# Kernel tuning notes

Measured on AMD Instinct MI355X. Metric: run time of the kernel, lower is better.

## Reference

```python
import jax, jax.numpy as jnp
import numpy as np

D_MODEL = 256; N_HEADS = 8; D_FF = 1024; N_LAYERS = 8; N_BLOCKS = 4
VOCAB = 10000; N_SPARSE = 26; N_DENSE = 13; BATCH = 4096
SEQ = N_DENSE + N_SPARSE  # 39 feature tokens


def _ln(x, g, b, eps=1e-5):
    m = jnp.mean(x, -1, keepdims=True)
    v = jnp.mean((x - m) ** 2, -1, keepdims=True)
    return (x - m) * jax.lax.rsqrt(v + eps) * g + b


def _normalize(x, axis=-1, eps=1e-12):
    n = jnp.maximum(jnp.linalg.norm(x, axis=axis, keepdims=True), eps)
    return x / n


def setup_inputs() -> dict:
    key = jax.random.key(0)
    ks = iter(jax.random.split(key, 64))
    d, L, ff = D_MODEL, N_LAYERS, D_FF
    w = lambda shape: jax.random.normal(next(ks), shape, dtype=jnp.float32) * 0.02
    z = lambda shape: jnp.zeros(shape, jnp.float32)
    o = lambda shape: jnp.ones(shape, jnp.float32)
    return {
        "dense_x": jax.random.normal(next(ks), (BATCH, N_DENSE), dtype=jnp.float32),
        "sparse_x": jax.random.randint(next(ks), (BATCH, N_SPARSE), 0, VOCAB, dtype=jnp.int32),
        "W_dense": w((N_DENSE * d, N_DENSE)), "b_dense": z((N_DENSE * d,)),
        "emb": w((N_SPARSE, VOCAB + 1, d)),
        "Wq": w((L, d, d)), "bq": z((L, d)),
        "Wk": w((L, d, d)), "bk": z((L, d)),
        "Wv": w((L, d, d)), "bv": z((L, d)),
        "W1": w((L, ff, d)), "b1": z((L, ff)),
        "W2": w((L, d, ff)), "b2": z((L, d)),
        "n1g": o((L, d)), "n1b": z((L, d)),
        "n2g": o((L, d)), "n2b": z((L, d)),
        "qvec": w((N_BLOCKS, d)),
        "mha_in_w": w((3 * d, d)), "mha_in_b": z((3 * d,)),
        "mha_out_w": w((d, d)), "mha_out_b": z((d,)),
        "ng": o((d,)), "ngb": z((d,)),
        "Wo1": w((D_FF, SEQ * d)), "bo1": z((D_FF,)),
        "Wo2": w((1, D_FF)), "bo2": z((1,)),
    }


def reference(dense_x, sparse_x, W_dense, b_dense, emb, Wq, bq, Wk, bk, Wv, bv,
              W1, b1, W2, b2, n1g, n1b, n2g, n2b, qvec,
              mha_in_w, mha_in_b, mha_out_w, mha_out_b, ng, ngb,
              Wo1, bo1, Wo2, bo2):
    B = dense_x.shape[0]; d = D_MODEL; H = N_HEADS; dh = d // H
    # --- embed_features ---
    dense_emb = (dense_x @ W_dense.T + b_dense).reshape(B, N_DENSE, d)
    emb0 = emb.at[:, 0, :].set(0.0)  # padding_idx=0
    sp = emb0[jnp.arange(N_SPARSE), sparse_x]  # [B, 26, d]
    x = jnp.concatenate([dense_emb, sp], axis=1)  # [B, 39, d]

    scale = 1.0 / jnp.sqrt(jnp.float32(d))  # note: d_model, not head_dim
    block_size = N_LAYERS // N_BLOCKS
    block_outputs = [x]
    for i in range(N_LAYERS):
        # --- HSTU layer: sigmoid pointwise attention ---
        r = x
        h = _ln(x, n1g[i], n1b[i])
        q = (h @ Wq[i].T + bq[i]).reshape(B, SEQ, H, dh).transpose(0, 2, 1, 3)
        k = (h @ Wk[i].T + bk[i]).reshape(B, SEQ, H, dh).transpose(0, 2, 1, 3)
        v = (h @ Wv[i].T + bv[i]).reshape(B, SEQ, H, dh).transpose(0, 2, 1, 3)
        aw = jax.nn.sigmoid(jnp.einsum('bhqd,bhkd->bhqk', q, k) * scale)
        ao = jnp.einsum('bhqk,bhkd->bhqd', aw, v).transpose(0, 2, 1, 3).reshape(B, SEQ, d)
        x = r + ao
        r = x
        h = _ln(x, n2g[i], n2b[i])
        x = r + (jax.nn.relu(h @ W1[i].T + b1[i]) @ W2[i].T + b2[i])
        # --- AttentionResidual block mixing ---
        if (i + 1) % block_size == 0 and i < N_LAYERS - 1:
            V = jnp.stack(block_outputs + [x])  # [n, B, T, d]
            K = _normalize(V)
            qi = min(len(block_outputs), N_BLOCKS - 1)
            qn = _normalize(qvec[qi], axis=0)
            logits = jnp.einsum('d,nbtd->nbt', qn, K)
            wt = jax.nn.softmax(logits, axis=0)
            x = jnp.einsum('nbt,nbtd->btd', wt, V)
            block_outputs.append(x)

    # --- final LayerNorm + standard MHA residual ---
    r = x
    h = _ln(x, ng, ngb)
    qkv = h @ mha_in_w.T + mha_in_b
    q, k, v = jnp.split(qkv, 3, axis=-1)
    q = q.reshape(B, SEQ, H, dh).transpose(0, 2, 1, 3)
    k = k.reshape(B, SEQ, H, dh).transpose(0, 2, 1, 3)
    v = v.reshape(B, SEQ, H, dh).transpose(0, 2, 1, 3)
    at = jax.nn.softmax(jnp.einsum('bhqd,bhkd->bhqk', q, k) / jnp.sqrt(jnp.float32(dh)), axis=-1)
    mo = jnp.einsum('bhqk,bhkd->bhqd', at, v).transpose(0, 2, 1, 3).reshape(B, SEQ, d)
    x = r + (mo @ mha_out_w.T + mha_out_b)

    flat = x.reshape(B, -1)
    return (jax.nn.relu(flat @ Wo1.T + bo1) @ Wo2.T + bo2).squeeze(-1)
```

## Files before the change

### kernel.cpp

```cpp
#include <hip/hip_runtime.h>
#include <hip/hip_bf16.h>

typedef __attribute__((ext_vector_type(4))) float f32x4;
typedef __attribute__((ext_vector_type(8))) short short8;
typedef __attribute__((ext_vector_type(4))) unsigned short us4;

static __device__ __forceinline__ unsigned short f2bf(float f){
  return __builtin_bit_cast(unsigned short, __float2bfloat16(f));
}
static __device__ __forceinline__ float bf2f(unsigned short u){
  return __bfloat162float(__builtin_bit_cast(__hip_bfloat16, u));
}
static __device__ __forceinline__ short8 zero8(){
  short8 v;
#pragma unroll
  for (int e=0;e<8;++e) v[e]=0;
  return v;
}
static __device__ __forceinline__ void g2l16(const void* g, void* l){
  __builtin_amdgcn_global_load_lds(
    (const __attribute__((address_space(1))) unsigned int*)g,
    (__attribute__((address_space(3))) unsigned int*)l, 16, 0, 0);
}

template<int EPI>
__global__ __launch_bounds__(256)
void gemm_k(const unsigned short* __restrict__ Ap, int lda,
            const unsigned short* __restrict__ Bp,
            const float* __restrict__ bias,
            void* __restrict__ Outp, int ldo, int K,
            unsigned short* __restrict__ vT, int nColBlk)
{
  const int id = blockIdx.x;
  const int xcd = id & 7; const int t0 = id >> 3;
  const int cb = t0 % nColBlk; const int rb = (t0 / nColBlk)*8 + xcd;
  const long rowBase = (long)rb << 7;
  const long colBase = (long)cb << 7;
  const int tid = threadIdx.x, lane = tid & 63, w = tid >> 6;
  const int wm = (w >> 1) << 6, wn = (w & 1) << 6;
  const int cl = lane & 15, q4 = lane >> 4;

  __shared__ __align__(16) unsigned short As[128*64];
  __shared__ __align__(16) unsigned short Bs[128*64];

  const char* bSrc[4]; unsigned short* bDst[4];
  const char* aSrc[4]; unsigned short* aDst[4];
#pragma unroll
  for (int g=0; g<4; ++g){
    const int c = (w<<8) + (g<<6) + lane;
    const int r = c>>3, x = c&7, c16 = x ^ (r&7);
    bSrc[g] = (const char*)(Bp + (colBase + r)*(long)K) + c16*16;
    bDst[g] = Bs + (((w<<2)+g)<<9);
    aSrc[g] = (const char*)(Ap + (rowBase + r)*(long)lda) + c16*16;
    aDst[g] = As + (((w<<2)+g)<<9);
  }

  f32x4 acc[4][4];
#pragma unroll
  for (int m=0;m<4;++m)
#pragma unroll
    for (int n=0;n<4;++n) acc[m][n] = (f32x4){0.f,0.f,0.f,0.f};

  const int nk = K >> 6;
  for (int t=0; t<nk; ++t){
    if (t) __syncthreads();
    const long tb = (long)t << 7;
#pragma unroll
    for (int g=0; g<4; ++g){
      g2l16(bSrc[g] + tb, bDst[g]);
      g2l16(aSrc[g] + tb, aDst[g]);
    }
    __syncthreads();
#pragma unroll
    for (int ks=0; ks<2; ++ks){
      const int kb = ks*64 + (q4<<4);
      short8 af[4], bf_[4];
#pragma unroll
      for (int m=0;m<4;++m){
        const int r = wm + m*16 + cl;
        af[m] = *(const short8*)((const char*)As + r*128 + (kb ^ ((r&7)<<4)));
      }
#pragma unroll
      for (int n=0;n<4;++n){
        const int r = wn + n*16 + cl;
        bf_[n] = *(const short8*)((const char*)Bs + r*128 + (kb ^ ((r&7)<<4)));
      }
#pragma unroll
      for (int m=0;m<4;++m)
#pragma unroll
        for (int n=0;n<4;++n)
          acc[m][n] = __builtin_amdgcn_mfma_f32_16x16x32_bf16(af[m], bf_[n], acc[m][n], 0,0,0);
    }
  }

#pragma unroll
  for (int n=0;n<4;++n){
    const long col = colBase + wn + n*16 + cl;
    const float bi = bias[col];
#pragma unroll
    for (int m=0;m<4;++m){
      const long r0 = rowBase + wm + m*16 + (q4<<2);
#pragma unroll
      for (int i=0;i<4;++i){
        const float v = acc[m][n][i] + bi;
        const long row = r0 + i;
        if constexpr (EPI == 1){
          ((unsigned short*)Outp)[row*(long)ldo + col] = f2bf(fmaxf(v,0.f));
        } else {
          if (col < 512){
            ((unsigned short*)Outp)[row*512 + col] = f2bf(v);
          } else {
            const int bb = (int)row / 39;
            const int tt = (int)row - bb*39;
            unsigned short* vrow = vT + ((long)bb*256 + (col - 512))*48;
            vrow[tt] = f2bf(v);
            if (tt < 9) vrow[tt + 39] = 0;
          }
        }
      }
    }
  }
}

__global__ __launch_bounds__(512)
void ffn_k(const float* __restrict__ xf_in,
           const float* __restrict__ sB, const float* __restrict__ cB,
           const unsigned short* __restrict__ W1p,
           const float* __restrict__ b1p,
           const unsigned short* __restrict__ W2p,
           const float* __restrict__ b2p,
           float* __restrict__ xf,
           unsigned short* __restrict__ xln1)
{
  __shared__ __align__(16) unsigned short Wb1[64*256];
  __shared__ __align__(16) unsigned short Wb2[256*64];
  __shared__ __align__(16) unsigned short Hs[128*64];
  float* part1 = (float*)Wb1;
  float* part2 = part1 + 512;
  float* sln   = part2 + 512;
  float* cln   = sln + 128;

  const int tid = threadIdx.x, lane = tid & 63, w = tid >> 6;
  const int cl = lane & 15, q4 = lane >> 4;
  const long rowBase = (long)blockIdx.x << 7;
  const int wm = (w >> 2) << 6, wn = (w & 3) << 6;

  short8 af[8];
  {
    const int row = (w<<4) + cl;
    const float s = sB[rowBase + row], c = cB[rowBase + row];
    const float* src = xf_in + (rowBase + row)*256 + (q4<<3);
#pragma unroll
    for (int kt=0; kt<8; ++kt){
      f32x4 a = *(const f32x4*)(src + kt*32);
      f32x4 b = *(const f32x4*)(src + kt*32 + 4);
      short8 v;
#pragma unroll
      for (int e=0;e<4;++e){ v[e] = (short)f2bf(a[e]*s + c); v[4+e] = (short)f2bf(b[e]*s + c); }
      af[kt] = v;
    }
  }

  f32x4 acc[4][4];
#pragma unroll
  for (int m=0;m<4;++m)
#pragma unroll
    for (int n=0;n<4;++n) acc[m][n] = (f32x4){0.f,0.f,0.f,0.f};

  for (int j=0; j<16; ++j){
    const int ffbase = j<<6;
    __syncthreads();
#pragma unroll
    for (int it=0; it<4; ++it){
      const int g = tid + (it<<9);
      {
        const int kt = g>>9, cc = g&511, rr = cc>>3, xs = cc&7;
        g2l16(W1p + ((long)(ffbase+rr))*256 + (kt<<6) + ((xs^(rr&7))<<3),
              Wb1 + (((tid & ~63) + (it<<9))<<3));
      }
      {
        const int rr = g>>3, xs = g&7;
        g2l16(W2p + (long)rr*1024 + ffbase + ((xs^(rr&7))<<3),
              Wb2 + (((tid & ~63) + (it<<9))<<3));
      }
    }
    float b1v[4];
#pragma unroll
    for (int n=0;n<4;++n) b1v[n] = b1p[ffbase + n*16 + cl];
    __syncthreads();

    f32x4 hacc[4];
#pragma unroll
    for (int n=0;n<4;++n) hacc[n] = (f32x4){0.f,0.f,0.f,0.f};
#pragma unroll
    for (int kt2=0; kt2<4; ++kt2)
#pragma unroll
      for (int ks=0; ks<2; ++ks){
        const int kb = ks*64 + (q4<<4);
        const short8 a = af[kt2*2 + ks];
#pragma unroll
        for (int n=0;n<4;++n){
          const int rn = n*16 + cl;
          short8 bf_ = *(const short8*)((const char*)Wb1 + (kt2<<13) + rn*128 + (kb ^ ((rn&7)<<4)));
          hacc[n] = __builtin_amdgcn_mfma_f32_16x16x32_bf16(a, bf_, hacc[n], 0,0,0);
        }
      }
#pragma unroll
    for (int n=0;n<4;++n)
#pragma unroll
      for (int i=0;i<4;++i){
        const int hr = (w<<4) + (q4<<2) + i, hc = n*16 + cl;
        const float hv = fmaxf(hacc[n][i] + b1v[n], 0.f);
        *(unsigned short*)((char*)Hs + hr*128 + ((hc*2) ^ ((hr&7)<<4))) = f2bf(hv);
      }
    __syncthreads();

#pragma unroll
    for (int ks=0; ks<2; ++ks){
      const int kb = ks*64 + (q4<<4);
      short8 am[4], bm[4];
#pragma unroll
      for (int m=0;m<4;++m){
        const int r = wm + m*16 + cl;
        am[m] = *(const short8*)((const char*)Hs + r*128 + (kb ^ ((r&7)<<4)));
      }
#pragma unroll
      for (int n=0;n<4;++n){
        const int r = wn + n*16 + cl;
        bm[n] = *(const short8*)((const char*)Wb2 + r*128 + (kb ^ ((r&7)<<4)));
      }
#pragma unroll
      for (int m=0;m<4;++m)
#pragma unroll
        for (int n=0;n<4;++n)
          acc[m][n] = __builtin_amdgcn_mfma_f32_16x16x32_bf16(am[m], bm[n], acc[m][n], 0,0,0);
    }
  }

#pragma unroll
  for (int n=0;n<4;++n){
    const int col = wn + n*16 + cl;
    const float bi = b2p[col];
#pragma unroll
    for (int m=0;m<4;++m)
#pragma unroll
      for (int i=0;i<4;++i){
        const int row = wm + m*16 + (q4<<2) + i;
        const long gi = (rowBase + row)*256 + col;
        const float v = acc[m][n][i] + bi + xf[gi];
        acc[m][n][i] = v;
        xf[gi] = v;
      }
  }
  __syncthreads();
#pragma unroll
  for (int m=0;m<4;++m)
#pragma unroll
    for (int i=0;i<4;++i){
      float s1 = 0.f, s2 = 0.f;
#pragma unroll
      for (int n=0;n<4;++n){ const float v = acc[m][n][i]; s1 += v; s2 += v*v; }
#pragma unroll
      for (int off=8; off; off>>=1){ s1 += __shfl_xor(s1, off, 16); s2 += __shfl_xor(s2, off, 16); }
      const int row = wm + m*16 + (q4<<2) + i;
      if (cl == 0){ part1[row*4 + (w&3)] = s1; part2[row*4 + (w&3)] = s2; }
    }
  __syncthreads();
  if (tid < 128){
    const float S1 = part1[tid*4]+part1[tid*4+1]+part1[tid*4+2]+part1[tid*4+3];
    const float S2 = part2[tid*4]+part2[tid*4+1]+part2[tid*4+2]+part2[tid*4+3];
    const float mn = S1*(1.f/256.f);
    const float var = S2*(1.f/256.f) - mn*mn;
    const float s = rsqrtf(var + 1e-5f);
    sln[tid] = s; cln[tid] = -mn*s;
  }
  __syncthreads();
#pragma unroll
  for (int m=0;m<4;++m)
#pragma unroll
    for (int i=0;i<4;++i){
      const int row = wm + m*16 + (q4<<2) + i;
      const float s = sln[row], c = cln[row];
#pragma unroll
      for (int n=0;n<4;++n){
        const int col = wn + n*16 + cl;
        xln1[(rowBase + row)*256 + col] = f2bf(acc[m][n][i]*s + c);
      }
    }
}

__global__ __launch_bounds__(256)
void attn_sig_k(const unsigned short* __restrict__ qkb,
                const unsigned short* __restrict__ vT,
                float* xf, float* __restrict__ sB, float* __restrict__ cB)
{
  __shared__ __align__(16) unsigned short Ps[4*48*64];
  __shared__ float part[312];

  const int b = blockIdx.x;
  const int tid = threadIdx.x, lane = tid & 63, w = tid >> 6;
  const int cl = lane & 15, q4 = lane >> 4;
  unsigned short* P = Ps + w*3072;
  const unsigned short* qb = qkb + (long)b*39*512;
  const unsigned short* vbb = vT + (long)b*256*48;

  if (lane < 48){
    const int r = lane;
    *(short8*)((char*)P + r*128 + (96  ^ ((r&7)<<4))) = zero8();
    *(short8*)((char*)P + r*128 + (112 ^ ((r&7)<<4))) = zero8();
  }

  float ps1[3][4], ps2[3][4];
#pragma unroll
  for (int m=0;m<3;++m)
#pragma unroll
    for (int i=0;i<4;++i){ ps1[m][i]=0.f; ps2[m][i]=0.f; }

#pragma unroll
  for (int hh=0; hh<2; ++hh){
    const int h = (w<<1) + hh;
    f32x4 sac[3][3];
#pragma unroll
    for (int m=0;m<3;++m)
#pragma unroll
      for (int n=0;n<3;++n) sac[m][n] = (f32x4){0.f,0.f,0.f,0.f};
    short8 aq[3], bk8[3];
#pragma unroll
    for (int m=0;m<3;++m){
      const int r = m*16 + cl;
      aq[m] = (r < 39) ? *(const short8*)(qb + (long)r*512 + h*32 + q4*8) : zero8();
    }
#pragma unroll
    for (int n=0;n<3;++n){
      const int r = n*16 + cl;
      bk8[n] = (r < 39) ? *(const short8*)(qb + (long)r*512 + 256 + h*32 + q4*8) : zero8();
    }
#pragma unroll
    for (int m=0;m<3;++m)
#pragma unroll
      for (int n=0;n<3;++n)
        sac[m][n] = __builtin_amdgcn_mfma_f32_16x16x32_bf16(aq[m], bk8[n], sac[m][n], 0,0,0);
#pragma unroll
    for (int m=0;m<3;++m)
#pragma unroll
      for (int n=0;n<3;++n)
#pragma unroll
        for (int i=0;i<4;++i){
          const int row = m*16 + (q4<<2) + i, col = n*16 + cl;
          const float pv = 1.f/(1.f + __expf(-sac[m][n][i]*0.0625f));
          *(unsigned short*)((char*)P + row*128 + ((col*2) ^ ((row&7)<<4))) = f2bf(pv);
        }
    f32x4 aoc[3][2];
#pragma unroll
    for (int m=0;m<3;++m)
#pragma unroll
      for (int n=0;n<2;++n) aoc[m][n] = (f32x4){0.f,0.f,0.f,0.f};
#pragma unroll
    for (int ks=0; ks<2; ++ks){
      const int kb = ks*64 + (q4<<4);
      short8 pa[3], vb[2];
#pragma unroll
      for (int m=0;m<3;++m){
        const int r = m*16 + cl;
        pa[m] = *(const short8*)((const char*)P + r*128 + (kb ^ ((r&7)<<4)));
      }
#pragma unroll
      for (int n=0;n<2;++n){
        vb[n] = zero8();
        if (ks == 0 || q4 < 2)
          vb[n] = *(const short8*)(vbb + (long)(h*32 + n*16 + cl)*48 + ks*32 + q4*8);
      }
#pragma unroll
      for (int m=0;m<3;++m)
#pragma unroll
        for (int n=0;n<2;++n)
          aoc[m][n] = __builtin_amdgcn_mfma_f32_16x16x32_bf16(pa[m], vb[n], aoc[m][n], 0,0,0);
    }
#pragma unroll
    for (int m=0;m<3;++m)
#pragma unroll
      for (int n=0;n<2;++n)
#pragma unroll
        for (int i=0;i<4;++i){
          const int row = m*16 + (q4<<2) + i;
          if (row < 39){
            const long gi = (((long)(b*39+row))<<8) + h*32 + n*16 + cl;
            const float nv = xf[gi] + aoc[m][n][i];
            xf[gi] = nv;
            ps1[m][i] += nv; ps2[m][i] += nv*nv;
          }
        }
  }
#pragma unroll
  for (int m=0;m<3;++m)
#pragma unroll
    for (int i=0;i<4;++i){
      float a1 = ps1[m][i], a2 = ps2[m][i];
#pragma unroll
      for (int off=8; off; off>>=1){ a1 += __shfl_xor(a1, off, 16); a2 += __shfl_xor(a2, off, 16); }
      const int row = m*16 + (q4<<2) + i;
      if (cl == 0 && row < 39){ part[row*8 + (w<<1)] = a1; part[row*8 + (w<<1) + 1] = a2; }
    }
  __syncthreads();
  if (tid < 39){
    const float S1 = part[tid*8]+part[tid*8+2]+part[tid*8+4]+part[tid*8+6];
    const float S2 = part[tid*8+1]+part[tid*8+3]+part[tid*8+5]+part[tid*8+7];
    const float mn = S1*(1.f/256.f);
    const float var = S2*(1.f/256.f) - mn*mn;
    const float s = rsqrtf(var + 1e-5f);
    sB[b*39+tid] = s; cB[b*39+tid] = -mn*s;
  }
}

__global__ __launch_bounds__(256)
void attn_fin_k(const unsigned short* __restrict__ qkb,
                const unsigned short* __restrict__ vT,
                const float* __restrict__ xf,
                const unsigned short* __restrict__ moW,
                const float* __restrict__ moB,
                unsigned short* __restrict__ flatb)
{
  __shared__ __align__(16) unsigned short Ps[4*48*64];
  __shared__ __align__(16) unsigned short Mo[48*256];

  const int b = blockIdx.x;
  const int tid = threadIdx.x, lane = tid & 63, w = tid >> 6;
  const int cl = lane & 15, q4 = lane >> 4;
  unsigned short* P = Ps + w*3072;
  const unsigned short* qb = qkb + (long)b*39*512;
  const unsigned short* vbb = vT + (long)b*256*48;
  const float SC = 0.17677669529663687f;

  if (lane < 48){
    const int r = lane;
    *(short8*)((char*)P + r*128 + (96  ^ ((r&7)<<4))) = zero8();
    *(short8*)((char*)P + r*128 + (112 ^ ((r&7)<<4))) = zero8();
  }

#pragma unroll
  for (int hh=0; hh<2; ++hh){
    const int h = (w<<1) + hh;
    f32x4 sac[3][3];
#pragma unroll
    for (int m=0;m<3;++m)
#pragma unroll
      for (int n=0;n<3;++n) sac[m][n] = (f32x4){0.f,0.f,0.f,0.f};
    short8 aq[3], bk8[3];
#pragma unroll
    for (int m=0;m<3;++m){
      const int r = m*16 + cl;
      aq[m] = (r < 39) ? *(const short8*)(qb + (long)r*512 + h*32 + q4*8) : zero8();
    }
#pragma unroll
    for (int n=0;n<3;++n){
      const int r = n*16 + cl;
      bk8[n] = (r < 39) ? *(const short8*)(qb + (long)r*512 + 256 + h*32 + q4*8) : zero8();
    }
#pragma unroll
    for (int m=0;m<3;++m)
#pragma unroll
      for (int n=0;n<3;++n)
        sac[m][n] = __builtin_amdgcn_mfma_f32_16x16x32_bf16(aq[m], bk8[n], sac[m][n], 0,0,0);
#pragma unroll
    for (int m=0;m<3;++m)
#pragma unroll
      for (int i=0;i<4;++i){
        const float v0 = sac[m][0][i]*SC, v1 = sac[m][1][i]*SC, v2 = sac[m][2][i]*SC;
        const bool c2ok = (32 + cl) < 39;
        float mx = fmaxf(v0, v1);
        if (c2ok) mx = fmaxf(mx, v2);
#pragma unroll
        for (int off=8; off; off>>=1) mx = fmaxf(mx, __shfl_xor(mx, off, 16));
        const float e0 = __expf(v0-mx), e1 = __expf(v1-mx);
        const float e2 = c2ok ? __expf(v2-mx) : 0.f;
        float s = e0+e1+e2;
#pragma unroll
        for (int off=8; off; off>>=1) s += __shfl_xor(s, off, 16);
        const float inv = 1.f/s;
        const int row = m*16 + (q4<<2) + i;
        *(unsigned short*)((char*)P + row*128 + (((cl   )*2) ^ ((row&7)<<4))) = f2bf(e0*inv);
        *(unsigned short*)((char*)P + row*128 + (((16+cl)*2) ^ ((row&7)<<4))) = f2bf(e1*inv);
        *(unsigned short*)((char*)P + row*128 + (((32+cl)*2) ^ ((row&7)<<4))) = f2bf(e2*inv);
      }
    f32x4 aoc[3][2];
#pragma unroll
    for (int m=0;m<3;++m)
#pragma unroll
      for (int n=0;n<2;++n) aoc[m][n] = (f32x4){0.f,0.f,0.f,0.f};
#pragma unroll
    for (int ks=0; ks<2; ++ks){
      const int kb = ks*64 + (q4<<4);
      short8 pa[3], vb[2];
#pragma unroll
      for (int m=0;m<3;++m){
        const int r = m*16 + cl;
        pa[m] = *(const short8*)((const char*)P + r*128 + (kb ^ ((r&7)<<4)));
      }
#pragma unroll
      for (int n=0;n<2;++n){
        vb[n] = zero8();
        if (ks == 0 || q4 < 2)
          vb[n] = *(const short8*)(vbb + (long)(h*32 + n*16 + cl)*48 + ks*32 + q4*8);
      }
#pragma unroll
      for (int m=0;m<3;++m)
#pragma unroll
        for (int n=0;n<2;++n)
          aoc[m][n] = __builtin_amdgcn_mfma_f32_16x16x32_bf16(pa[m], vb[n], aoc[m][n], 0,0,0);
    }
#pragma unroll
    for (int m=0;m<3;++m)
#pragma unroll
      for (int n=0;n<2;++n)
#pragma unroll
        for (int i=0;i<4;++i){
          const int row = m*16 + (q4<<2) + i;
          const int colq = h*32 + n*16 + cl;
          *(unsigned short*)((char*)Mo + row*512 + ((colq*2) ^ ((row&7)<<4))) = f2bf(aoc[m][n][i]);
        }
  }
  __syncthreads();
  f32x4 oc[3][4];
#pragma unroll
  for (int m=0;m<3;++m)
#pragma unroll
    for (int n=0;n<4;++n) oc[m][n] = (f32x4){0.f,0.f,0.f,0.f};
#pragma unroll
  for (int ks=0; ks<8; ++ks){
    const int kb = ks*64 + (q4<<4);
    short8 am[3], bm[4];
#pragma unroll
    for (int m=0;m<3;++m){
      const int r = m*16 + cl;
      am[m] = *(const short8*)((const char*)Mo + r*512 + (kb ^ ((r&7)<<4)));
    }
#pragma unroll
    for (int n=0;n<4;++n){
      const int nn = (w<<6) + n*16 + cl;
      bm[n] = *(const short8*)(moW + (long)nn*256 + ks*32 + q4*8);
    }
#pragma unroll
    for (int m=0;m<3;++m)
#pragma unroll
      for (int n=0;n<4;++n)
        oc[m][n] = __builtin_amdgcn_mfma_f32_16x16x32_bf16(am[m], bm[n], oc[m][n], 0,0,0);
  }
#pragma unroll
  for (int m=0;m<3;++m)
#pragma unroll
    for (int n=0;n<4;++n)
#pragma unroll
      for (int i=0;i<4;++i){
        const int row = m*16 + (q4<<2) + i;
        if (row < 39){
          const int col = (w<<6) + n*16 + cl;
          const float v = oc[m][n][i] + moB[col] + xf[(((long)(b*39+row))<<8) + col];
          flatb[(long)b*9984 + row*256 + col] = f2bf(v);
        }
      }
}

__global__ __launch_bounds__(256)
void embed_k(const float* __restrict__ dense_x, const int* __restrict__ sparse_x,
             const float* __restrict__ W_dense, const float* __restrict__ b_dense,
             const float* __restrict__ emb,
             float* __restrict__ xf, unsigned short* __restrict__ x0b,
             unsigned short* __restrict__ xln1)
{
  const int bid = blockIdx.x;
  const int b = bid / 39, t = bid - b*39;
  const int c = threadIdx.x;
  float v;
  if (t < 13){
    const int j = t*256 + c;
    v = b_dense[j];
    const float* wr = W_dense + (long)j*13;
    const float* dx = dense_x + (long)b*13;
#pragma unroll
    for (int k2=0;k2<13;++k2) v = fmaf(dx[k2], wr[k2], v);
  } else {
    const int idx = sparse_x[b*26 + (t-13)];
    v = (idx == 0) ? 0.f : emb[((long)(t-13)*10001 + idx)*256 + c];
  }
  const long row = bid;
  xf[row*256 + c] = v;
  x0b[row*256 + c] = f2bf(v);
  float s1 = v, s2 = v*v;
#pragma unroll
  for (int off=32; off; off>>=1){ s1 += __shfl_xor(s1, off); s2 += __shfl_xor(s2, off); }
  __shared__ float r1[4], r2[4];
  const int lane = c & 63, wq = c >> 6;
  if (lane == 0){ r1[wq]=s1; r2[wq]=s2; }
  __syncthreads();
  const float S1 = r1[0]+r1[1]+r1[2]+r1[3];
  const float S2 = r2[0]+r2[1]+r2[2]+r2[3];
  const float mn = S1*(1.f/256.f);
  const float var = S2*(1.f/256.f) - mn*mn;
  const float s = rsqrtf(var+1e-5f);
  xln1[row*256 + c] = f2bf((v - mn)*s);
}

template<int NSRC>
__global__ __launch_bounds__(256)
void mix_k(float* __restrict__ xf,
           const unsigned short* __restrict__ s0,
           const unsigned short* __restrict__ s1p,
           const unsigned short* __restrict__ s2p,
           unsigned short* mout,
           const float* __restrict__ qvec, int qi,
           unsigned short* __restrict__ xln1)
{
  const int b = blockIdx.x;
  const int tid = threadIdx.x, lane = tid&63, w = tid>>6;
  const int c4 = lane << 2;
  f32x4 q = *(const f32x4*)(qvec + qi*256 + c4);
  float qq = q[0]*q[0]+q[1]*q[1]+q[2]*q[2]+q[3]*q[3];
#pragma unroll
  for (int off=32; off; off>>=1) qq += __shfl_xor(qq, off);
  const float qsc = 1.f/fmaxf(sqrtf(qq), 1e-12f);
#pragma unroll
  for (int e=0;e<4;++e) q[e] *= qsc;
  for (int t = w; t < 39; t += 4){
    const long ro = ((long)(b*39+t))*256 + c4;
    f32x4 v[NSRC];
#pragma unroll
    for (int n=0;n<NSRC;++n){
      if (n == NSRC-1) v[n] = *(const f32x4*)(xf + ro);
      else {
        const unsigned short* sp = (n==0)?s0:((n==1)?s1p:s2p);
        us4 u = *(const us4*)(sp + ro);
#pragma unroll
        for (int e=0;e<4;++e) v[n][e] = bf2f(u[e]);
      }
    }
    float lg[NSRC];
#pragma unroll
    for (int n=0;n<NSRC;++n){
      float nn = v[n][0]*v[n][0]+v[n][1]*v[n][1]+v[n][2]*v[n][2]+v[n][3]*v[n][3];
      float dd = q[0]*v[n][0]+q[1]*v[n][1]+q[2]*v[n][2]+q[3]*v[n][3];
#pragma unroll
      for (int off=32; off; off>>=1){ nn += __shfl_xor(nn,off); dd += __shfl_xor(dd,off); }
      lg[n] = dd / fmaxf(sqrtf(nn), 1e-12f);
    }
    float mx = lg[0];
#pragma unroll
    for (int n=1;n<NSRC;++n) mx = fmaxf(mx, lg[n]);
    float es = 0.f, e_[NSRC];
#pragma unroll
    for (int n=0;n<NSRC;++n){ e_[n] = __expf(lg[n]-mx); es += e_[n]; }
    const float inv = 1.f/es;
    f32x4 o = {0.f,0.f,0.f,0.f};
#pragma unroll
    for (int n=0;n<NSRC;++n){
      const float wt = e_[n]*inv;
#pragma unroll
      for (int e=0;e<4;++e) o[e] = fmaf(wt, v[n][e], o[e]);
    }
    *(f32x4*)(xf + ro) = o;
    if (mout){
      us4 u;
#pragma unroll
      for (int e=0;e<4;++e) u[e] = f2bf(o[e]);
      *(us4*)(mout + ro) = u;
    }
    float s1 = o[0]+o[1]+o[2]+o[3];
    float s2 = o[0]*o[0]+o[1]*o[1]+o[2]*o[2]+o[3]*o[3];
#pragma unroll
    for (int off=32; off; off>>=1){ s1 += __shfl_xor(s1,off); s2 += __shfl_xor(s2,off); }
    const float mn = s1*(1.f/256.f);
    const float var = s2*(1.f/256.f)-mn*mn;
    const float s = rsqrtf(var+1e-5f);
    const float c = -mn*s;
    us4 u2;
#pragma unroll
    for (int e=0;e<4;++e) u2[e] = f2bf(o[e]*s + c);
    *(us4*)(xln1 + ro) = u2;
  }
}

__global__ __launch_bounds__(256)
void head2_k(const unsigned short* __restrict__ h1h, const float* __restrict__ Wo2,
             const float* __restrict__ bo2, float* __restrict__ outp)
{
  const int b = blockIdx.x*4 + (threadIdx.x>>6);
  const int lane = threadIdx.x & 63;
  float s = 0.f;
#pragma unroll
  for (int g=0; g<2; ++g){
    const int base = lane*16 + g*8;
    short8 v8 = *(const short8*)(h1h + (long)b*1024 + base);
#pragma unroll
    for (int e=0;e<8;++e) s = fmaf(bf2f((unsigned short)v8[e]), Wo2[base+e], s);
  }
#pragma unroll
  for (int off=32; off; off>>=1) s += __shfl_xor(s, off);
  if (lane==0) outp[b] = s + bo2[0];
}

__global__ void cvt_k(const float* __restrict__ src, unsigned short* __restrict__ dst, long n){
  const long i = (long)blockIdx.x*256 + threadIdx.x;
  if (i < n) dst[i] = f2bf(src[i]);
}
__global__ void prep_qkv_k(const float* Wq, const float* Wk, const float* Wv,
                           const float* g, unsigned short* dst){
  const int n = blockIdx.x, i = blockIdx.y, k = threadIdx.x;
  const int sel = n >> 8, nn = n & 255;
  const float* W = sel==0?Wq:(sel==1?Wk:Wv);
  dst[((long)i*768 + n)*256 + k] = f2bf(W[((long)i*256+nn)*256 + k] * g[i*256+k]);
}
__global__ void prep_qkvb_k(const float* Wq,const float* Wk,const float* Wv,
                            const float* bq,const float* bk,const float* bv,
                            const float* beta, float* dst){
  const int n = blockIdx.x, i = blockIdx.y, k = threadIdx.x;
  const int sel = n>>8, nn = n&255;
  const float* W = sel==0?Wq:(sel==1?Wk:Wv);
  const float* bb = sel==0?bq:(sel==1?bk:bv);
  float v = beta[i*256+k] * W[((long)i*256+nn)*256+k];
  __shared__ float r[4];
#pragma unroll
  for (int off=32; off; off>>=1) v += __shfl_xor(v, off);
  if ((k&63)==0) r[k>>6] = v;
  __syncthreads();
  if (k==0) dst[i*768+n] = bb[i*256+nn] + r[0]+r[1]+r[2]+r[3];
}
__global__ void prep_w1_k(const float* W1, const float* g, unsigned short* dst){
  const int n = blockIdx.x, i = blockIdx.y, k = threadIdx.x;
  const long o = ((long)i*1024+n)*256 + k;
  dst[o] = f2bf(W1[o] * g[i*256+k]);
}
__global__ void prep_w1b_k(const float* W1, const float* b1, const float* beta, float* dst){
  const int n = blockIdx.x, i = blockIdx.y, k = threadIdx.x;
  float v = beta[i*256+k] * W1[((long)i*1024+n)*256+k];
  __shared__ float r[4];
#pragma unroll
  for (int off=32; off; off>>=1) v += __shfl_xor(v, off);
  if ((k&63)==0) r[k>>6] = v;
  __syncthreads();
  if (k==0) dst[i*1024+n] = b1[i*1024+n] + r[0]+r[1]+r[2]+r[3];
}
__global__ void prep_mha_k(const float* W, const float* g, unsigned short* dst){
  const int n = blockIdx.x, k = threadIdx.x;
  dst[n*256+k] = f2bf(W[n*256+k]*g[k]);
}
__global__ void prep_mhab_k(const float* W, const float* bb, const float* beta, float* dst){
  const int n = blockIdx.x, k = threadIdx.x;
  float v = beta[k]*W[n*256+k];
  __shared__ float r[4];
#pragma unroll
  for (int off=32; off; off>>=1) v += __shfl_xor(v, off);
  if ((k&63)==0) r[k>>6] = v;
  __syncthreads();
  if (k==0) dst[n] = bb[n] + r[0]+r[1]+r[2]+r[3];
}

extern "C" void kernel_launch(void* const* d_in, const int* in_sizes, int n_in,
                              void* d_out, int out_size, void* d_ws, size_t ws_size,
                              hipStream_t stream)
{
  (void)in_sizes; (void)n_in; (void)out_size; (void)ws_size;
  const float* dense_x  = (const float*)d_in[0];
  const int*   sparse_x = (const int*)d_in[1];
  const float* W_dense  = (const float*)d_in[2];
  const float* b_dense  = (const float*)d_in[3];
  const float* emb      = (const float*)d_in[4];
  const float* Wq = (const float*)d_in[5];
  const float* bq = (const float*)d_in[6];
  const float* Wk = (const float*)d_in[7];
  const float* bk = (const float*)d_in[8];
  const float* Wv = (const float*)d_in[9];
  const float* bv = (const float*)d_in[10];
  const float* W1 = (const float*)d_in[11];
  const float* b1 = (const float*)d_in[12];
  const float* W2 = (const float*)d_in[13];
  const float* b2 = (const float*)d_in[14];
  const float* n1g= (const float*)d_in[15];
  const float* n1b= (const float*)d_in[16];
  const float* n2g= (const float*)d_in[17];
  const float* n2b= (const float*)d_in[18];
  const float* qvec=(const float*)d_in[19];
  const float* mha_in_w = (const float*)d_in[20];
  const float* mha_in_b = (const float*)d_in[21];
  const float* mha_out_w= (const float*)d_in[22];
  const float* mha_out_b= (const float*)d_in[23];
  const float* ng = (const float*)d_in[24];
  const float* ngb= (const float*)d_in[25];
  const float* Wo1= (const float*)d_in[26];
  const float* bo1= (const float*)d_in[27];
  const float* Wo2= (const float*)d_in[28];
  const float* bo2= (const float*)d_in[29];

  char* ws = (char*)d_ws;
  size_t off = 0;
  auto alloc = [&](size_t bytes)->void*{ void* p = ws + off; off += (bytes + 255) & ~(size_t)255; return p; };
  float* xf            = (float*)alloc(163577856ull);
  unsigned short* qkh  = (unsigned short*)alloc(163577856ull);
  unsigned short* vT   = (unsigned short*)alloc(100663296ull);
  unsigned short* x0b  = (unsigned short*)alloc(81788928ull);
  unsigned short* m1b  = (unsigned short*)alloc(81788928ull);
  unsigned short* m2b  = (unsigned short*)alloc(81788928ull);
  unsigned short* xln1 = (unsigned short*)alloc(81788928ull);
  unsigned short* h1h  = (unsigned short*)alloc(8388608ull);
  float* sB = (float*)alloc(638976ull);
  float* cB = (float*)alloc(638976ull);
  unsigned short* Wqkv_f = (unsigned short*)alloc(3145728ull);
  float* bqkv_f = (float*)alloc(24576ull);
  unsigned short* W1_f = (unsigned short*)alloc(4194304ull);
  float* b1_f = (float*)alloc(32768ull);
  unsigned short* W2_f = (unsigned short*)alloc(4194304ull);
  unsigned short* mhain_f = (unsigned short*)alloc(393216ull);
  float* mhainb_f = (float*)alloc(3072ull);
  unsigned short* mhaout_f = (unsigned short*)alloc(131072ull);
  unsigned short* Wo1_f = (unsigned short*)alloc(20447232ull);

  unsigned short* flatb = m1b;

  cvt_k<<<8192,256,0,stream>>>(W2, W2_f, 2097152L);
  cvt_k<<<256,256,0,stream>>>(mha_out_w, mhaout_f, 65536L);
  cvt_k<<<39936,256,0,stream>>>(Wo1, Wo1_f, 10223616L);
  prep_qkv_k<<<dim3(768,8),256,0,stream>>>(Wq,Wk,Wv,n1g,Wqkv_f);
  prep_qkvb_k<<<dim3(768,8),256,0,stream>>>(Wq,Wk,Wv,bq,bk,bv,n1b,bqkv_f);
  prep_w1_k<<<dim3(1024,8),256,0,stream>>>(W1,n2g,W1_f);
  prep_w1b_k<<<dim3(1024,8),256,0,stream>>>(W1,b1,n2b,b1_f);
  prep_mha_k<<<768,256,0,stream>>>(mha_in_w, ng, mhain_f);
  prep_mhab_k<<<768,256,0,stream>>>(mha_in_w, mha_in_b, ngb, mhainb_f);

  embed_k<<<159744,256,0,stream>>>(dense_x, sparse_x, W_dense, b_dense, emb, xf, x0b, xln1);

  for (int i = 0; i < 8; ++i){
    gemm_k<3><<<7488,256,0,stream>>>(xln1, 256,
        Wqkv_f + (size_t)i*196608, bqkv_f + i*768, qkh, 512, 256, vT, 6);
    attn_sig_k<<<4096,256,0,stream>>>(qkh, vT, xf, sB, cB);
    ffn_k<<<1248,512,0,stream>>>(xf, sB, cB,
        W1_f + (size_t)i*262144, b1_f + i*1024,
        W2_f + (size_t)i*262144, b2 + i*256, xf, xln1);
    if (i == 1)      mix_k<2><<<4096,256,0,stream>>>(xf, x0b, m1b, m2b, m1b, qvec, 1, xln1);
    else if (i == 3) mix_k<3><<<4096,256,0,stream>>>(xf, x0b, m1b, m2b, m2b, qvec, 2, xln1);
    else if (i == 5) mix_k<4><<<4096,256,0,stream>>>(xf, x0b, m1b, m2b, nullptr, qvec, 3, xln1);
  }
  gemm_k<3><<<7488,256,0,stream>>>(xln1, 256, mhain_f, mhainb_f, qkh, 512, 256, vT, 6);
  attn_fin_k<<<4096,256,0,stream>>>(qkh, vT, xf, mhaout_f, mha_out_b, flatb);
  gemm_k<1><<<256,256,0,stream>>>(flatb, 9984, Wo1_f, bo1, h1h, 1024, 9984, nullptr, 8);
  head2_k<<<1024,256,0,stream>>>(h1h, Wo2, bo2, (float*)d_out);
}
```

Measured before the change: 6.924 ms.

## Halve FFN row tile to 64 and read W2 fragments directly from global

The fused FFN kernel now processes 64 rows per block with 256 threads instead of 128 rows with 512 threads, doubling the grid. The W2 tile is no longer staged through LDS. Each wave loads its B fragments straight from global memory, which frees LDS and may raise occupancy. The cost is that W1 reuse per block is halved and W2 reads become uncoalesced per-lane global loads repeated by every block.

Measured after the change: 8.830 ms. 1.28x slower.

```diff
diff --git a/kernel.cpp b/kernel.cpp
--- a/kernel.cpp
+++ b/kernel.cpp
@@ -122,7 +122,7 @@
   }
 }
 
-__global__ __launch_bounds__(512)
+__global__ __launch_bounds__(256)
 void ffn_k(const float* __restrict__ xf_in,
            const float* __restrict__ sB, const float* __restrict__ cB,
            const unsigned short* __restrict__ W1p,
@@ -133,17 +133,15 @@
            unsigned short* __restrict__ xln1)
 {
   __shared__ __align__(16) unsigned short Wb1[64*256];
-  __shared__ __align__(16) unsigned short Wb2[256*64];
-  __shared__ __align__(16) unsigned short Hs[128*64];
+  __shared__ __align__(16) unsigned short Hs[64*64];
   float* part1 = (float*)Wb1;
-  float* part2 = part1 + 512;
-  float* sln   = part2 + 512;
-  float* cln   = sln + 128;
+  float* part2 = part1 + 256;
+  float* sln   = part2 + 256;
+  float* cln   = sln + 64;
 
   const int tid = threadIdx.x, lane = tid & 63, w = tid >> 6;
   const int cl = lane & 15, q4 = lane >> 4;
-  const long rowBase = (long)blockIdx.x << 7;
-  const int wm = (w >> 2) << 6, wn = (w & 3) << 6;
+  const long rowBase = (long)blockIdx.x << 6;
 
   short8 af[8];
   {
@@ -171,18 +169,11 @@
     const int ffbase = j<<6;
     __syncthreads();
 #pragma unroll
-    for (int it=0; it<4; ++it){
-      const int g = tid + (it<<9);
-      {
-        const int kt = g>>9, cc = g&511, rr = cc>>3, xs = cc&7;
-        g2l16(W1p + ((long)(ffbase+rr))*256 + (kt<<6) + ((xs^(rr&7))<<3),
-              Wb1 + (((tid & ~63) + (it<<9))<<3));
-      }
-      {
-        const int rr = g>>3, xs = g&7;
-        g2l16(W2p + (long)rr*1024 + ffbase + ((xs^(rr&7))<<3),
-              Wb2 + (((tid & ~63) + (it<<9))<<3));
-      }
+    for (int it=0; it<8; ++it){
+      const int c = (it<<8) + (w<<6) + lane;
+      const int kt = c>>9, cc = c&511, rr = cc>>3, xs = cc&7;
+      g2l16(W1p + ((long)(ffbase+rr))*256 + (kt<<6) + ((xs^(rr&7))<<3),
+            Wb1 + (((it<<8) + (w<<6))<<3));
     }
     float b1v[4];
 #pragma unroll
@@ -221,13 +212,13 @@
       short8 am[4], bm[4];
 #pragma unroll
       for (int m=0;m<4;++m){
-        const int r = wm + m*16 + cl;
+        const int r = m*16 + cl;
         am[m] = *(const short8*)((const char*)Hs + r*128 + (kb ^ ((r&7)<<4)));
       }
 #pragma unroll
       for (int n=0;n<4;++n){
-        const int r = wn + n*16 + cl;
-        bm[n] = *(const short8*)((const char*)Wb2 + r*128 + (kb ^ ((r&7)<<4)));
+        const long rr = (w<<6) + n*16 + cl;
+        bm[n] = *(const short8*)(W2p + rr*1024 + ffbase + ks*32 + (q4<<3));
       }
 #pragma unroll
       for (int m=0;m<4;++m)
@@ -239,13 +230,13 @@
 
 #pragma unroll
   for (int n=0;n<4;++n){
-    const int col = wn + n*16 + cl;
+    const int col = (w<<6) + n*16 + cl;
     const float bi = b2p[col];
 #pragma unroll
     for (int m=0;m<4;++m)
 #pragma unroll
       for (int i=0;i<4;++i){
-        const int row = wm + m*16 + (q4<<2) + i;
+        const int row = m*16 + (q4<<2) + i;
         const long gi = (rowBase + row)*256 + col;
         const float v = acc[m][n][i] + bi + xf[gi];
         acc[m][n][i] = v;
@@ -262,11 +253,11 @@
       for (int n=0;n<4;++n){ const float v = acc[m][n][i]; s1 += v; s2 += v*v; }
 #pragma unroll
       for (int off=8; off; off>>=1){ s1 += __shfl_xor(s1, off, 16); s2 += __shfl_xor(s2, off, 16); }
-      const int row = wm + m*16 + (q4<<2) + i;
-      if (cl == 0){ part1[row*4 + (w&3)] = s1; part2[row*4 + (w&3)] = s2; }
+      const int row = m*16 + (q4<<2) + i;
+      if (cl == 0){ part1[row*4 + w] = s1; part2[row*4 + w] = s2; }
     }
   __syncthreads();
-  if (tid < 128){
+  if (tid < 64){
     const float S1 = part1[tid*4]+part1[tid*4+1]+part1[tid*4+2]+part1[tid*4+3];
     const float S2 = part2[tid*4]+part2[tid*4+1]+part2[tid*4+2]+part2[tid*4+3];
     const float mn = S1*(1.f/256.f);
@@ -279,11 +270,11 @@
   for (int m=0;m<4;++m)
 #pragma unroll
     for (int i=0;i<4;++i){
-      const int row = wm + m*16 + (q4<<2) + i;
+      const int row = m*16 + (q4<<2) + i;
       const float s = sln[row], c = cln[row];
 #pragma unroll
       for (int n=0;n<4;++n){
-        const int col = wn + n*16 + cl;
+        const int col = (w<<6) + n*16 + cl;
         xln1[(rowBase + row)*256 + col] = f2bf(acc[m][n][i]*s + c);
       }
     }
@@ -830,7 +821,7 @@
     gemm_k<3><<<7488,256,0,stream>>>(xln1, 256,
         Wqkv_f + (size_t)i*196608, bqkv_f + i*768, qkh, 512, 256, vT, 6);
     attn_sig_k<<<4096,256,0,stream>>>(qkh, vT, xf, sB, cB);
-    ffn_k<<<1248,512,0,stream>>>(xf, sB, cB,
+    ffn_k<<<2496,256,0,stream>>>(xf, sB, cB,
         W1_f + (size_t)i*262144, b1_f + i*1024,
         W2_f + (size_t)i*262144, b2 + i*256, xf, xln1);
     if (i == 1)      mix_k<2><<<4096,256,0,stream>>>(xf, x0b, m1b, m2b, m1b, qvec, 1, xln1);
```

## Add dedicated QKV GEMM kernel keeping full A row-tile resident in LDS

Applied to the files above, without the earlier changes.

Replaces the generic tiled GEMM for the QKV projections with a kernel that loads a 128x256 A tile into LDS once and loops over all six 128-column output blocks. B fragments are read directly from global memory instead of being staged through LDS. This cuts redundant A loads and the block count per launch, but the 64KB of LDS lowers occupancy and there is no pipelining of the B reads. The generic GEMM is reduced to its ReLU epilogue only.

Measured after the change: 7.046 ms. Within noise of the previous version (+1.8%).

```diff
diff --git a/kernel.cpp b/kernel.cpp
--- a/kernel.cpp
+++ b/kernel.cpp
@@ -23,13 +23,88 @@
     (__attribute__((address_space(3))) unsigned int*)l, 16, 0, 0);
 }
 
-template<int EPI>
+__global__ __launch_bounds__(256)
+void qkv_k(const unsigned short* __restrict__ Ap,
+           const unsigned short* __restrict__ Bp,
+           const float* __restrict__ bias,
+           unsigned short* __restrict__ qk,
+           unsigned short* __restrict__ vT)
+{
+  __shared__ __align__(16) unsigned short As[128*256];
+
+  const int tid = threadIdx.x, lane = tid & 63, w = tid >> 6;
+  const int cl = lane & 15, q4 = lane >> 4;
+  const long rowBase = (long)blockIdx.x << 7;
+  const int wm = (w >> 1) << 6, wn = (w & 1) << 6;
+
+#pragma unroll
+  for (int it=0; it<16; ++it){
+    const int c = (it<<8) + (w<<6) + lane;
+    const int kt = c>>10, rem = c & 1023, r = rem>>3, x = rem&7;
+    g2l16(Ap + (rowBase + r)*256 + (kt<<6) + (((x ^ (r&7)))<<3),
+          As + (((it<<8) + (w<<6))<<3));
+  }
+  __syncthreads();
+
+  for (int cb=0; cb<6; ++cb){
+    f32x4 acc[4][4];
+#pragma unroll
+    for (int m=0;m<4;++m)
+#pragma unroll
+      for (int n=0;n<4;++n) acc[m][n] = (f32x4){0.f,0.f,0.f,0.f};
+#pragma unroll
+    for (int kt=0; kt<4; ++kt)
+#pragma unroll
+      for (int ks=0; ks<2; ++ks){
+        const int kb = ks*64 + (q4<<4);
+        short8 af[4], bf_[4];
+#pragma unroll
+        for (int m=0;m<4;++m){
+          const int r = wm + m*16 + cl;
+          af[m] = *(const short8*)((const char*)As + (kt<<14) + r*128 + (kb ^ ((r&7)<<4)));
+        }
+#pragma unroll
+        for (int n=0;n<4;++n){
+          const long rn = cb*128 + wn + n*16 + cl;
+          bf_[n] = *(const short8*)(Bp + rn*256 + (kt<<6) + ks*32 + (q4<<3));
+        }
+#pragma unroll
+        for (int m=0;m<4;++m)
+#pragma unroll
+          for (int n=0;n<4;++n)
+            acc[m][n] = __builtin_amdgcn_mfma_f32_16x16x32_bf16(af[m], bf_[n], acc[m][n], 0,0,0);
+      }
+#pragma unroll
+    for (int n=0;n<4;++n){
+      const int col = cb*128 + wn + n*16 + cl;
+      const float bi = bias[col];
+#pragma unroll
+      for (int m=0;m<4;++m){
+        const long r0 = rowBase + wm + m*16 + (q4<<2);
+#pragma unroll
+        for (int i=0;i<4;++i){
+          const float v = acc[m][n][i] + bi;
+          const long row = r0 + i;
+          if (col < 512){
+            qk[row*512 + col] = f2bf(v);
+          } else {
+            const int bb = (int)row / 39;
+            const int tt = (int)row - bb*39;
+            unsigned short* vrow = vT + ((long)bb*256 + (col - 512))*48;
+            vrow[tt] = f2bf(v);
+            if (tt < 9) vrow[tt + 39] = 0;
+          }
+        }
+      }
+    }
+  }
+}
+
 __global__ __launch_bounds__(256)
 void gemm_k(const unsigned short* __restrict__ Ap, int lda,
             const unsigned short* __restrict__ Bp,
             const float* __restrict__ bias,
-            void* __restrict__ Outp, int ldo, int K,
-            unsigned short* __restrict__ vT, int nColBlk)
+            unsigned short* __restrict__ Outp, int ldo, int K, int nColBlk)
 {
   const int id = blockIdx.x;
   const int xcd = id & 7; const int t0 = id >> 3;
@@ -103,20 +178,7 @@
 #pragma unroll
       for (int i=0;i<4;++i){
         const float v = acc[m][n][i] + bi;
-        const long row = r0 + i;
-        if constexpr (EPI == 1){
-          ((unsigned short*)Outp)[row*(long)ldo + col] = f2bf(fmaxf(v,0.f));
-        } else {
-          if (col < 512){
-            ((unsigned short*)Outp)[row*512 + col] = f2bf(v);
-          } else {
-            const int bb = (int)row / 39;
-            const int tt = (int)row - bb*39;
-            unsigned short* vrow = vT + ((long)bb*256 + (col - 512))*48;
-            vrow[tt] = f2bf(v);
-            if (tt < 9) vrow[tt + 39] = 0;
-          }
-        }
+        Outp[(r0+i)*(long)ldo + col] = f2bf(fmaxf(v,0.f));
       }
     }
   }
@@ -827,8 +889,7 @@
   embed_k<<<159744,256,0,stream>>>(dense_x, sparse_x, W_dense, b_dense, emb, xf, x0b, xln1);
 
   for (int i = 0; i < 8; ++i){
-    gemm_k<3><<<7488,256,0,stream>>>(xln1, 256,
-        Wqkv_f + (size_t)i*196608, bqkv_f + i*768, qkh, 512, 256, vT, 6);
+    qkv_k<<<1248,256,0,stream>>>(xln1, Wqkv_f + (size_t)i*196608, bqkv_f + i*768, qkh, vT);
     attn_sig_k<<<4096,256,0,stream>>>(qkh, vT, xf, sB, cB);
     ffn_k<<<1248,512,0,stream>>>(xf, sB, cB,
         W1_f + (size_t)i*262144, b1_f + i*1024,
@@ -837,8 +898,8 @@
     else if (i == 3) mix_k<3><<<4096,256,0,stream>>>(xf, x0b, m1b, m2b, m2b, qvec, 2, xln1);
     else if (i == 5) mix_k<4><<<4096,256,0,stream>>>(xf, x0b, m1b, m2b, nullptr, qvec, 3, xln1);
   }
-  gemm_k<3><<<7488,256,0,stream>>>(xln1, 256, mhain_f, mhainb_f, qkh, 512, 256, vT, 6);
+  qkv_k<<<1248,256,0,stream>>>(xln1, mhain_f, mhainb_f, qkh, vT);
   attn_fin_k<<<4096,256,0,stream>>>(qkh, vT, xf, mhaout_f, mha_out_b, flatb);
-  gemm_k<1><<<256,256,0,stream>>>(flatb, 9984, Wo1_f, bo1, h1h, 1024, 9984, nullptr, 8);
+  gemm_k<<<256,256,0,stream>>>(flatb, 9984, Wo1_f, bo1, h1h, 1024, 9984, 8);
   head2_k<<<1024,256,0,stream>>>(h1h, Wo2, bo2, (float*)d_out);
 }
```
